# Kernel optimization log

Hardware: AMD Instinct MI355X
Metric: run time of the kernel (lower is better)

## Reference

```python
import jax, jax.numpy as jnp
import numpy as np

NUM_HEADS = 16
LN_EPS = 1e-6

B, S, D, INTER = 16, 729, 1152, 4304


def setup_inputs() -> dict:
    key = jax.random.key(0)
    ks = jax.random.split(key, 8)
    std = 0.02
    return {
        "hidden_state": jax.random.normal(ks[0], (B, S, D), jnp.float32),
        "probe": jax.random.normal(ks[1], (1, 1, D), jnp.float32),
        "in_proj_weight": jax.random.normal(ks[2], (3 * D, D), jnp.float32) * std,
        "in_proj_bias": jax.random.normal(ks[3], (3 * D,), jnp.float32) * std,
        "ln_weight": jnp.ones((D,), jnp.float32),
        "ln_bias": jnp.zeros((D,), jnp.float32),
        "fc1_w": jax.random.normal(ks[4], (INTER, D), jnp.float32) * std,
        "fc1_b": jnp.zeros((INTER,), jnp.float32),
        "fc2_w": jax.random.normal(ks[5], (D, INTER), jnp.float32) * std,
        "fc2_b": jnp.zeros((D,), jnp.float32),
    }


def reference(hidden_state, probe, in_proj_weight, in_proj_bias,
              ln_weight, ln_bias, fc1_w, fc1_b, fc2_w, fc2_b):
    b, s, d = hidden_state.shape
    h = NUM_HEADS
    hd = d // h
    Wq, Wk, Wv = in_proj_weight[:d], in_proj_weight[d:2 * d], in_proj_weight[2 * d:]
    bq, bk, bv = in_proj_bias[:d], in_proj_bias[d:2 * d], in_proj_bias[2 * d:]

    # Projections (F.linear: x @ W.T + b)
    q = jnp.broadcast_to(probe, (b, 1, d)) @ Wq.T + bq          # [b,1,d]
    k = hidden_state @ Wk.T + bk                                 # [b,s,d]
    v = hidden_state @ Wv.T + bv                                 # [b,s,d] (this is the 'value' the head keeps)

    # Single-query attention scores per head; embed splits to (h, hd)
    qh = q.reshape(b, h, hd) / jnp.sqrt(jnp.asarray(hd, q.dtype))  # [b,h,hd]
    kh = k.reshape(b, s, h, hd)                                    # [b,s,h,hd]
    scores = jnp.einsum('bhd,bshd->bhs', qh, kh)                   # [b,h,s]
    attn_weights = jax.nn.softmax(scores, axis=-1)                 # [b,h,s]
    # NOTE: original module computes attn_output + out_proj but discards them.

    # Residual MLP on value
    mu = jnp.mean(v, axis=-1, keepdims=True)
    var = jnp.var(v, axis=-1, keepdims=True)
    vn = (v - mu) / jnp.sqrt(var + LN_EPS) * ln_weight + ln_bias
    mlp = jax.nn.gelu(vn @ fc1_w.T + fc1_b, approximate=True) @ fc2_w.T + fc2_b
    out = v + mlp                                                  # [b,s,d]
    return out, attn_weights
```

## Files before the change

### kernel.cpp

```cpp
#include <hip/hip_runtime.h>
#include <hip/hip_bf16.h>

typedef __bf16 bf16;
typedef __bf16 bf16x4 __attribute__((ext_vector_type(4)));
typedef __bf16 bf16x8 __attribute__((ext_vector_type(8)));
typedef float f32x4 __attribute__((ext_vector_type(4)));

#define NB 16
#define NS 729
#define ND 1152
#define NDP 1280
#define NH 16
#define NHD 72
#define NI 4304
#define NM (NB*NS)
#define MP 11776
#define NIP 4352
#define OUT0 ((size_t)NM*(size_t)ND)
#define LNEPS 1e-6f

#define GLOAD16(gp, lp) __builtin_amdgcn_global_load_lds( \
    (const __attribute__((address_space(1))) void*)(gp),  \
    (__attribute__((address_space(3))) void*)(lp), 16, 0, 0)

static __device__ __forceinline__ void nt_store_f32(float v, float* p) {
  __builtin_nontemporal_store(v, p);
}

__global__ __launch_bounds__(256) void k_conv_w(const float* __restrict__ src,
                                                bf16* __restrict__ dst,
                                                int sR, int sC, int dR, int dC) {
  int idx = blockIdx.x * 256 + threadIdx.x;
  int rowlen = dC >> 2;
  int r = idx / rowlen;
  int c = (idx - r * rowlen) * 4;
  if (r >= dR) return;
  bf16x4 o;
  if (r < sR && c + 4 <= sC) {
    float4 v = *(const float4*)(&src[(size_t)r * sC + c]);
    o[0] = (bf16)v.x; o[1] = (bf16)v.y; o[2] = (bf16)v.z; o[3] = (bf16)v.w;
  } else {
    o[0] = (bf16)0.f; o[1] = (bf16)0.f; o[2] = (bf16)0.f; o[3] = (bf16)0.f;
  }
  *(bf16x4*)(&dst[(size_t)r * dC + c]) = o;
}

__global__ __launch_bounds__(256) void k_pad(bf16* __restrict__ dst) {
  int idx = blockIdx.x * 256 + threadIdx.x;
  bf16x4 z;
  z[0] = (bf16)0.f; z[1] = (bf16)0.f; z[2] = (bf16)0.f; z[3] = (bf16)0.f;
  *(bf16x4*)(&dst[(size_t)NM * ND + (size_t)idx * 4]) = z;
}

__global__ __launch_bounds__(256) void k_q(const float* __restrict__ Wq,
                                           const float* __restrict__ probe,
                                           const float* __restrict__ bq,
                                           float* __restrict__ q) {
  int d = blockIdx.x;
  const float* wrow = Wq + (size_t)d * ND;
  float s = 0.f;
  for (int e = threadIdx.x; e < ND; e += 256) s += wrow[e] * probe[e];
  for (int o = 32; o; o >>= 1) s += __shfl_down(s, o, 64);
  __shared__ float sm[4];
  if ((threadIdx.x & 63) == 0) sm[threadIdx.x >> 6] = s;
  __syncthreads();
  if (threadIdx.x == 0) q[d] = sm[0] + sm[1] + sm[2] + sm[3] + bq[d];
}

__global__ __launch_bounds__(256) void k_qk(const float* __restrict__ Wk,
                                            const float* __restrict__ bk,
                                            const float* __restrict__ q,
                                            float* __restrict__ qk,
                                            float* __restrict__ qb) {
  int idx = blockIdx.x * 256 + threadIdx.x;
  if (idx >= NH * ND) return;
  int h = idx / ND, e = idx - h * ND;
  const float scale = 0.11785113019775793f;
  float s = 0.f;
  for (int j = 0; j < NHD; ++j)
    s += q[h * NHD + j] * Wk[(size_t)(h * NHD + j) * ND + e];
  qk[idx] = s * scale;
  if (e == 0) {
    float sb = 0.f;
    for (int j = 0; j < NHD; ++j) sb += q[h * NHD + j] * bk[h * NHD + j];
    qb[h] = sb * scale;
  }
}

__global__ __launch_bounds__(256) void k_scores(const float* __restrict__ hs,
                                                const float* __restrict__ qk,
                                                const float* __restrict__ qb,
                                                float* __restrict__ attn,
                                                bf16* __restrict__ hsb) {
  int p = blockIdx.x;
  int t = threadIdx.x;
  const float* row = hs + (size_t)p * ND;
  bf16* orow = hsb + (size_t)p * ND;
  float acc[NH];
#pragma unroll
  for (int h = 0; h < NH; ++h) acc[h] = 0.f;
  for (int e = t; e < ND; e += 256) {
    float x = row[e];
    orow[e] = (bf16)x;
#pragma unroll
    for (int h = 0; h < NH; ++h) acc[h] += x * qk[h * ND + e];
  }
#pragma unroll
  for (int h = 0; h < NH; ++h)
    for (int o = 32; o; o >>= 1) acc[h] += __shfl_down(acc[h], o, 64);
  __shared__ float part[4][NH];
  int w = t >> 6, l = t & 63;
  if (l == 0) {
#pragma unroll
    for (int h = 0; h < NH; ++h) part[w][h] = acc[h];
  }
  __syncthreads();
  if (t < NH) {
    float s = part[0][t] + part[1][t] + part[2][t] + part[3][t] + qb[t];
    int b = p / NS, si = p - b * NS;
    attn[((size_t)(b * NH + t)) * NS + si] = s;
  }
}

__global__ __launch_bounds__(256) void k_softmax(float* __restrict__ attn) {
  float* a = attn + (size_t)blockIdx.x * NS;
  int t = threadIdx.x;
  float x0 = (t < NS) ? a[t] : -1e30f;
  float x1 = (t + 256 < NS) ? a[t + 256] : -1e30f;
  float x2 = (t + 512 < NS) ? a[t + 512] : -1e30f;
  float mx = fmaxf(x0, fmaxf(x1, x2));
  for (int o = 32; o; o >>= 1) mx = fmaxf(mx, __shfl_down(mx, o, 64));
  __shared__ float sm[4], sm2[4];
  if ((t & 63) == 0) sm[t >> 6] = mx;
  __syncthreads();
  mx = fmaxf(fmaxf(sm[0], sm[1]), fmaxf(sm[2], sm[3]));
  float e0 = (t < NS) ? __expf(x0 - mx) : 0.f;
  float e1 = (t + 256 < NS) ? __expf(x1 - mx) : 0.f;
  float e2 = (t + 512 < NS) ? __expf(x2 - mx) : 0.f;
  float s = e0 + e1 + e2;
  for (int o = 32; o; o >>= 1) s += __shfl_down(s, o, 64);
  if ((t & 63) == 0) sm2[t >> 6] = s;
  __syncthreads();
  float inv = 1.f / (sm2[0] + sm2[1] + sm2[2] + sm2[3]);
  if (t < NS) a[t] = e0 * inv;
  if (t + 256 < NS) a[t + 256] = e1 * inv;
  if (t + 512 < NS) a[t + 512] = e2 * inv;
}

__global__ __launch_bounds__(256) void k_ln(const float* __restrict__ v,
                                            const float* __restrict__ lw,
                                            const float* __restrict__ lb,
                                            bf16* __restrict__ vn) {
  int r = blockIdx.x;
  int t = threadIdx.x;
  if (r >= NM) {
    for (int c = t; c < ND; c += 256) vn[(size_t)r * ND + c] = (bf16)0.f;
    return;
  }
  const float* row = v + (size_t)r * ND;
  float s = 0.f, sq = 0.f;
  for (int c = t; c < ND; c += 256) {
    float x = row[c];
    s += x; sq += x * x;
  }
  for (int o = 32; o; o >>= 1) {
    s += __shfl_down(s, o, 64);
    sq += __shfl_down(sq, o, 64);
  }
  __shared__ float smS[4], smQ[4];
  if ((t & 63) == 0) { smS[t >> 6] = s; smQ[t >> 6] = sq; }
  __syncthreads();
  s = smS[0] + smS[1] + smS[2] + smS[3];
  sq = smQ[0] + smQ[1] + smQ[2] + smQ[3];
  float mu = s * (1.f / ND);
  float var = sq * (1.f / ND) - mu * mu;
  float rstd = rsqrtf(var + LNEPS);
  for (int c = t; c < ND; c += 256) {
    float x = row[c];
    vn[(size_t)r * ND + c] = (bf16)((x - mu) * rstd * lw[c] + lb[c]);
  }
}

template <int MODE>
__global__ __launch_bounds__(512, 2) void gemm256(const bf16* __restrict__ A,
                                                  const bf16* __restrict__ Bm,
                                                  const float* __restrict__ bias,
                                                  const float* __restrict__ resid,
                                                  float* __restrict__ Cf,
                                                  bf16* __restrict__ Cb,
                                                  int K, int Mreal, int Nreal,
                                                  int ldc, int gx, int G) {
  __shared__ bf16 lds[2][2][256 * 64];
  const int tid = threadIdx.x;
  const int w = tid >> 6, lane = tid & 63;

  const int nwg = gridDim.x;
  const int orig = blockIdx.x;
  const int qq = nwg >> 3, rr = nwg & 7;
  const int xcd = orig & 7, idx0 = orig >> 3;
  const int wgid = (xcd < rr ? xcd * (qq + 1) : rr * (qq + 1) + (xcd - rr) * qq) + idx0;

  const int gy = nwg / gx;
  const int full = (gy / G) * G * gx;
  int bx, by;
  if (wgid < full) {
    int g = wgid / (G * gx), r2 = wgid - g * (G * gx);
    bx = r2 / G; by = g * G + (r2 - bx * G);
  } else {
    int r2 = wgid - full;
    int base = (gy / G) * G, rows = gy - base;
    bx = r2 / rows; by = base + (r2 - bx * rows);
  }
  const int row0 = by * 256, col0 = bx * 256;

  const int laneRow = lane >> 3;
  const int laneChunk = (lane & 7) ^ laneRow;

  auto STAGE_A = [&](int buf, int half, int kt) {
#pragma unroll
    for (int j = 0; j < 2; ++j) {
      int rowb = half * 128 + (w * 2 + j) * 8;
      const bf16* gp = A + (size_t)(row0 + rowb + laneRow) * K + kt * 64 + laneChunk * 8;
      GLOAD16(gp, &lds[buf][0][rowb * 64]);
    }
  };
  auto STAGE_B = [&](int buf, int half, int kt) {
#pragma unroll
    for (int j = 0; j < 2; ++j) {
      int rowb = half * 128 + (w * 2 + j) * 8;
      const bf16* gp = Bm + (size_t)(col0 + rowb + laneRow) * K + kt * 64 + laneChunk * 8;
      GLOAD16(gp, &lds[buf][1][rowb * 64]);
    }
  };

  const int wm = w >> 2, wn = w & 3;
  const int fr = lane & 15, fq = lane >> 4;

  f32x4 acc[8][4] = {};

  const int nk = K >> 6;
  STAGE_A(0, 0, 0); STAGE_A(0, 1, 0);
  STAGE_B(0, 0, 0); STAGE_B(0, 1, 0);
  if (nk > 1) {
    STAGE_B(1, 0, 1); STAGE_B(1, 1, 1);
    asm volatile("s_waitcnt vmcnt(4)" ::: "memory");
  } else {
    asm volatile("s_waitcnt vmcnt(0)" ::: "memory");
  }
  __builtin_amdgcn_s_barrier();

  int cur = 0;
  for (int t = 0; t < nk; ++t) {
    const bf16* As = &lds[cur][0][0];
    const bf16* Bs = &lds[cur][1][0];
    bf16x8 bfr[4][2];
#pragma unroll
    for (int p = 0; p < 4; ++p) {
      if (p == 0) {
#pragma unroll
        for (int ni = 0; ni < 4; ++ni)
#pragma unroll
          for (int kk = 0; kk < 2; ++kk) {
            int r = wn * 64 + ni * 16 + fr;
            bfr[ni][kk] = *(const bf16x8*)(&Bs[r * 64 + ((kk * 4 + fq) ^ (fr & 7)) * 8]);
          }
      }
      bf16x8 af[2][2];
#pragma unroll
      for (int mm = 0; mm < 2; ++mm)
#pragma unroll
        for (int kk = 0; kk < 2; ++kk) {
          int r = wm * 128 + (p * 2 + mm) * 16 + fr;
          af[mm][kk] = *(const bf16x8*)(&As[r * 64 + ((kk * 4 + fq) ^ (fr & 7)) * 8]);
        }
      if (p == 0)      { if (t + 1 < nk) STAGE_A(cur ^ 1, 0, t + 1); }
      else if (p == 1) { if (t + 1 < nk) STAGE_A(cur ^ 1, 1, t + 1); }
      else if (p == 2) { if (t + 2 < nk) STAGE_B(cur, 0, t + 2); }
      else             { if (t + 2 < nk) STAGE_B(cur, 1, t + 2); }
      __builtin_amdgcn_s_barrier();
      __builtin_amdgcn_s_setprio(1);
#pragma unroll
      for (int mm = 0; mm < 2; ++mm)
#pragma unroll
        for (int ni = 0; ni < 4; ++ni) {
          acc[p * 2 + mm][ni] = __builtin_amdgcn_mfma_f32_16x16x32_bf16(
              af[mm][0], bfr[ni][0], acc[p * 2 + mm][ni], 0, 0, 0);
          acc[p * 2 + mm][ni] = __builtin_amdgcn_mfma_f32_16x16x32_bf16(
              af[mm][1], bfr[ni][1], acc[p * 2 + mm][ni], 0, 0, 0);
        }
      __builtin_amdgcn_s_setprio(0);
      if (p == 3 && t + 1 < nk) {
        if (t + 2 < nk) { asm volatile("s_waitcnt vmcnt(4)" ::: "memory"); }
        else            { asm volatile("s_waitcnt vmcnt(0)" ::: "memory"); }
      }
      __builtin_amdgcn_s_barrier();
    }
    cur ^= 1;
  }

  const int rb = row0 + wm * 128, cb = col0 + wn * 64;
#pragma unroll
  for (int mi = 0; mi < 8; ++mi) {
#pragma unroll
    for (int ni = 0; ni < 4; ++ni) {
      int c = cb + ni * 16 + fr;
#pragma unroll
      for (int j = 0; j < 4; ++j) {
        int r = rb + mi * 16 + fq * 4 + j;
        float v = acc[mi][ni][j];
        if (MODE == 0) {
          if (r < Mreal && c < Nreal) nt_store_f32(v + bias[c], &Cf[(size_t)r * ldc + c]);
        } else if (MODE == 1) {
          float g = 0.f;
          if (c < Nreal) {
            float x = v + bias[c];
            float z = 1.5957691216057308f * (x + 0.044715f * x * x * x);
            g = x / (1.f + __expf(-z));
          }
          Cb[(size_t)r * ldc + c] = (bf16)g;
        } else {
          if (r < Mreal && c < Nreal)
            nt_store_f32(v + bias[c] + resid[(size_t)r * ldc + c],
                         &Cf[(size_t)r * ldc + c]);
        }
      }
    }
  }
}

extern "C" void kernel_launch(void* const* d_in, const int* in_sizes, int n_in,
                              void* d_out, int out_size, void* d_ws, size_t ws_size,
                              hipStream_t stream) {
  const float* hs    = (const float*)d_in[0];
  const float* probe = (const float*)d_in[1];
  const float* ipw   = (const float*)d_in[2];
  const float* ipb   = (const float*)d_in[3];
  const float* lw    = (const float*)d_in[4];
  const float* lb    = (const float*)d_in[5];
  const float* fc1w  = (const float*)d_in[6];
  const float* fc1b  = (const float*)d_in[7];
  const float* fc2w  = (const float*)d_in[8];
  const float* fc2b  = (const float*)d_in[9];
  float* out  = (float*)d_out;
  float* attn = out + OUT0;

  char* ws = (char*)d_ws;
  size_t off = 0;
  auto alloc = [&](size_t bytes) {
    char* p = ws + off;
    off += (bytes + 255) & ~(size_t)255;
    return p;
  };
  float* q  = (float*)alloc((size_t)ND * 4);
  float* qk = (float*)alloc((size_t)NH * ND * 4);
  float* qb = (float*)alloc((size_t)NH * 4);
  bf16* hsb = (bf16*)alloc((size_t)MP * ND * 2);
  bf16* wvb = (bf16*)alloc((size_t)NDP * ND * 2);
  bf16* f1b = (bf16*)alloc((size_t)NIP * ND * 2);
  bf16* f2b = (bf16*)alloc((size_t)NDP * NIP * 2);
  bf16* vnb = (bf16*)alloc((size_t)MP * ND * 2);
  bf16* h1b = (bf16*)alloc((size_t)MP * NIP * 2);

  k_conv_w<<<(NDP * (ND / 4) + 255) / 256, 256, 0, stream>>>(
      ipw + (size_t)2 * ND * ND, wvb, ND, ND, NDP, ND);
  k_conv_w<<<(NIP * (ND / 4) + 255) / 256, 256, 0, stream>>>(
      fc1w, f1b, NI, ND, NIP, ND);
  k_conv_w<<<(NDP * (NIP / 4) + 255) / 256, 256, 0, stream>>>(
      fc2w, f2b, ND, NI, NDP, NIP);

  k_q<<<ND, 256, 0, stream>>>(ipw, probe, ipb, q);
  k_qk<<<(NH * ND + 255) / 256, 256, 0, stream>>>(
      ipw + (size_t)ND * ND, ipb + ND, q, qk, qb);
  k_scores<<<NM, 256, 0, stream>>>(hs, qk, qb, attn, hsb);
  k_pad<<<((MP - NM) * ND / 4) / 256, 256, 0, stream>>>(hsb);
  k_softmax<<<NB * NH, 256, 0, stream>>>(attn);

  gemm256<0><<<(MP / 256) * (NDP / 256), 512, 0, stream>>>(
      hsb, wvb, ipb + 2 * ND, nullptr, out, nullptr, ND, NM, ND, ND, NDP / 256, 4);
  k_ln<<<MP, 256, 0, stream>>>(out, lw, lb, vnb);
  gemm256<1><<<(MP / 256) * (NIP / 256), 512, 0, stream>>>(
      vnb, f1b, fc1b, nullptr, nullptr, h1b, ND, MP, NI, NIP, NIP / 256, 4);
  gemm256<2><<<(MP / 256) * (NDP / 256), 512, 0, stream>>>(
      h1b, f2b, fc2b, out, out, nullptr, NIP, NM, ND, ND, NDP / 256, 2);
}
```

Baseline: 534.9 us.

## Replace 256x256x64 GEMM tile with 128x256x32 tile and simpler double buffering

Rewrites the bf16 MFMA GEMM to use a 128x256 output tile with a 32-wide K step, a smaller LDS footprint (48KB vs 128KB) and launch bounds allowing more resident waves. The staggered 4-phase prefetch pipeline is replaced by a straightforward double buffer with a full vmcnt(0) wait every K step. The grid doubles, which helps load balance and occupancy, but halves per-tile arithmetic intensity and increases global traffic and barrier frequency.

```diff
diff --git a/kernel.cpp b/kernel.cpp
--- a/kernel.cpp
+++ b/kernel.cpp
@@ -182,7 +182,7 @@
 }
 
 template <int MODE>
-__global__ __launch_bounds__(512, 2) void gemm256(const bf16* __restrict__ A,
+__global__ __launch_bounds__(512, 4) void gemm128(const bf16* __restrict__ A,
                                                   const bf16* __restrict__ Bm,
                                                   const float* __restrict__ bias,
                                                   const float* __restrict__ resid,
@@ -190,7 +190,7 @@
                                                   bf16* __restrict__ Cb,
                                                   int K, int Mreal, int Nreal,
                                                   int ldc, int gx, int G) {
-  __shared__ bf16 lds[2][2][256 * 64];
+  __shared__ bf16 lds[2][384 * 32];
   const int tid = threadIdx.x;
   const int w = tid >> 6, lane = tid & 63;
 
@@ -211,96 +211,64 @@
     int base = (gy / G) * G, rows = gy - base;
     bx = r2 / rows; by = base + (r2 - bx * rows);
   }
-  const int row0 = by * 256, col0 = bx * 256;
-
-  const int laneRow = lane >> 3;
-  const int laneChunk = (lane & 7) ^ laneRow;
-
-  auto STAGE_A = [&](int buf, int half, int kt) {
-#pragma unroll
-    for (int j = 0; j < 2; ++j) {
-      int rowb = half * 128 + (w * 2 + j) * 8;
-      const bf16* gp = A + (size_t)(row0 + rowb + laneRow) * K + kt * 64 + laneChunk * 8;
-      GLOAD16(gp, &lds[buf][0][rowb * 64]);
-    }
+  const int row0 = by * 128, col0 = bx * 256;
+
+  const int laneRow = lane >> 2;
+  const int laneChunk = (lane & 3) ^ ((lane >> 3) & 3);
+
+  auto STAGE_A = [&](int buf, int kt) {
+    const bf16* gp = A + (size_t)(row0 + w * 16 + laneRow) * K + kt * 32 + laneChunk * 8;
+    GLOAD16(gp, &lds[buf][(w * 16) * 32]);
   };
-  auto STAGE_B = [&](int buf, int half, int kt) {
-#pragma unroll
-    for (int j = 0; j < 2; ++j) {
-      int rowb = half * 128 + (w * 2 + j) * 8;
-      const bf16* gp = Bm + (size_t)(col0 + rowb + laneRow) * K + kt * 64 + laneChunk * 8;
-      GLOAD16(gp, &lds[buf][1][rowb * 64]);
-    }
+  auto STAGE_B = [&](int buf, int u, int kt) {
+    const bf16* gp = Bm + (size_t)(col0 + u * 128 + w * 16 + laneRow) * K + kt * 32 + laneChunk * 8;
+    GLOAD16(gp, &lds[buf][4096 + (u * 128 + w * 16) * 32]);
   };
 
   const int wm = w >> 2, wn = w & 3;
   const int fr = lane & 15, fq = lane >> 4;
-
-  f32x4 acc[8][4] = {};
-
-  const int nk = K >> 6;
-  STAGE_A(0, 0, 0); STAGE_A(0, 1, 0);
-  STAGE_B(0, 0, 0); STAGE_B(0, 1, 0);
-  if (nk > 1) {
-    STAGE_B(1, 0, 1); STAGE_B(1, 1, 1);
-    asm volatile("s_waitcnt vmcnt(4)" ::: "memory");
-  } else {
-    asm volatile("s_waitcnt vmcnt(0)" ::: "memory");
-  }
+  const int fsw = ((fq ^ ((fr >> 1) & 3)) << 3);
+  const int arow = wm * 64 + fr;
+  const int brow = wn * 64 + fr;
+
+  f32x4 acc[4][4] = {};
+
+  const int nk = K >> 5;
+  STAGE_A(0, 0); STAGE_B(0, 0, 0); STAGE_B(0, 1, 0);
+  asm volatile("s_waitcnt vmcnt(0)" ::: "memory");
   __builtin_amdgcn_s_barrier();
 
   int cur = 0;
   for (int t = 0; t < nk; ++t) {
-    const bf16* As = &lds[cur][0][0];
-    const bf16* Bs = &lds[cur][1][0];
-    bf16x8 bfr[4][2];
-#pragma unroll
-    for (int p = 0; p < 4; ++p) {
-      if (p == 0) {
-#pragma unroll
-        for (int ni = 0; ni < 4; ++ni)
-#pragma unroll
-          for (int kk = 0; kk < 2; ++kk) {
-            int r = wn * 64 + ni * 16 + fr;
-            bfr[ni][kk] = *(const bf16x8*)(&Bs[r * 64 + ((kk * 4 + fq) ^ (fr & 7)) * 8]);
-          }
-      }
-      bf16x8 af[2][2];
-#pragma unroll
-      for (int mm = 0; mm < 2; ++mm)
-#pragma unroll
-        for (int kk = 0; kk < 2; ++kk) {
-          int r = wm * 128 + (p * 2 + mm) * 16 + fr;
-          af[mm][kk] = *(const bf16x8*)(&As[r * 64 + ((kk * 4 + fq) ^ (fr & 7)) * 8]);
-        }
-      if (p == 0)      { if (t + 1 < nk) STAGE_A(cur ^ 1, 0, t + 1); }
-      else if (p == 1) { if (t + 1 < nk) STAGE_A(cur ^ 1, 1, t + 1); }
-      else if (p == 2) { if (t + 2 < nk) STAGE_B(cur, 0, t + 2); }
-      else             { if (t + 2 < nk) STAGE_B(cur, 1, t + 2); }
-      __builtin_amdgcn_s_barrier();
-      __builtin_amdgcn_s_setprio(1);
-#pragma unroll
-      for (int mm = 0; mm < 2; ++mm)
-#pragma unroll
-        for (int ni = 0; ni < 4; ++ni) {
-          acc[p * 2 + mm][ni] = __builtin_amdgcn_mfma_f32_16x16x32_bf16(
-              af[mm][0], bfr[ni][0], acc[p * 2 + mm][ni], 0, 0, 0);
-          acc[p * 2 + mm][ni] = __builtin_amdgcn_mfma_f32_16x16x32_bf16(
-              af[mm][1], bfr[ni][1], acc[p * 2 + mm][ni], 0, 0, 0);
-        }
-      __builtin_amdgcn_s_setprio(0);
-      if (p == 3 && t + 1 < nk) {
-        if (t + 2 < nk) { asm volatile("s_waitcnt vmcnt(4)" ::: "memory"); }
-        else            { asm volatile("s_waitcnt vmcnt(0)" ::: "memory"); }
-      }
-      __builtin_amdgcn_s_barrier();
+    const bf16* As = &lds[cur][0];
+    const bf16* Bs = &lds[cur][4096];
+    if (t + 1 < nk) {
+      STAGE_A(cur ^ 1, t + 1);
+      STAGE_B(cur ^ 1, 0, t + 1);
+      STAGE_B(cur ^ 1, 1, t + 1);
     }
+    bf16x8 bfr[4];
+#pragma unroll
+    for (int ni = 0; ni < 4; ++ni)
+      bfr[ni] = *(const bf16x8*)(&Bs[(brow + ni * 16) * 32 + fsw]);
+    __builtin_amdgcn_s_setprio(1);
+#pragma unroll
+    for (int mi = 0; mi < 4; ++mi) {
+      bf16x8 af = *(const bf16x8*)(&As[(arow + mi * 16) * 32 + fsw]);
+#pragma unroll
+      for (int ni = 0; ni < 4; ++ni)
+        acc[mi][ni] = __builtin_amdgcn_mfma_f32_16x16x32_bf16(af, bfr[ni],
+                                                              acc[mi][ni], 0, 0, 0);
+    }
+    __builtin_amdgcn_s_setprio(0);
+    if (t + 1 < nk) { asm volatile("s_waitcnt vmcnt(0)" ::: "memory"); }
+    __builtin_amdgcn_s_barrier();
     cur ^= 1;
   }
 
-  const int rb = row0 + wm * 128, cb = col0 + wn * 64;
-#pragma unroll
-  for (int mi = 0; mi < 8; ++mi) {
+  const int rb = row0 + wm * 64, cb = col0 + wn * 64;
+#pragma unroll
+  for (int mi = 0; mi < 4; ++mi) {
 #pragma unroll
     for (int ni = 0; ni < 4; ++ni) {
       int c = cb + ni * 16 + fr;
@@ -375,11 +343,11 @@
   k_pad<<<((MP - NM) * ND / 4) / 256, 256, 0, stream>>>(hsb);
   k_softmax<<<NB * NH, 256, 0, stream>>>(attn);
 
-  gemm256<0><<<(MP / 256) * (NDP / 256), 512, 0, stream>>>(
-      hsb, wvb, ipb + 2 * ND, nullptr, out, nullptr, ND, NM, ND, ND, NDP / 256, 4);
+  gemm128<0><<<(MP / 128) * (NDP / 256), 512, 0, stream>>>(
+      hsb, wvb, ipb + 2 * ND, nullptr, out, nullptr, ND, NM, ND, ND, NDP / 256, 8);
   k_ln<<<MP, 256, 0, stream>>>(out, lw, lb, vnb);
-  gemm256<1><<<(MP / 256) * (NIP / 256), 512, 0, stream>>>(
-      vnb, f1b, fc1b, nullptr, nullptr, h1b, ND, MP, NI, NIP, NIP / 256, 4);
-  gemm256<2><<<(MP / 256) * (NDP / 256), 512, 0, stream>>>(
+  gemm128<1><<<(MP / 128) * (NIP / 256), 512, 0, stream>>>(
+      vnb, f1b, fc1b, nullptr, nullptr, h1b, ND, MP, NI, NIP, NIP / 256, 8);
+  gemm128<2><<<(MP / 128) * (NDP / 256), 512, 0, stream>>>(
       h1b, f2b, fc2b, out, out, nullptr, NIP, NM, ND, ND, NDP / 256, 2);
 }
```

Result: faster. 498.3 us (-6.8%).
